# Kernel optimization log

Measured on AMD Instinct MI355X. Metric: run time of the kernel, lower is better.

## Reference

```python
import jax, jax.numpy as jnp
import numpy as np

B = 8          # batch_size
N = 2048       # N_particles
D_SP = 2       # spatial dims
D = 16         # D_SP + hidden_dim
K = 32         # max_num_neighbors
R = 0.08       # neighbor_radius
DT = 0.01      # leapfrog step
BIG = 1e9


def setup_inputs() -> dict:
    key = jax.random.key(0)
    ks = jax.random.split(key, 8)
    H, C = 64, 32
    # node state: small random hidden features, deterministic disk positions
    x = jax.random.normal(ks[0], (B * N, D), dtype=jnp.float32) * 0.001
    i = jnp.arange(N, dtype=jnp.float32)
    golden = jnp.pi * (3.0 - jnp.sqrt(5.0))
    theta = i * golden
    r = 0.6 * jnp.sqrt((i + 0.5) / N)
    pos = jnp.stack([r * jnp.cos(theta), r * jnp.sin(theta)], axis=1)  # [N,2]
    pos = jnp.tile(pos, (B, 1)) + 0.01 * jax.random.normal(ks[1], (B * N, 2), dtype=jnp.float32)
    x = x.at[:, :D_SP].set(pos)
    W1 = jax.random.normal(ks[2], (2 * D, H), dtype=jnp.float32) * (1.0 / np.sqrt(2 * D))
    b1 = jnp.zeros((H,), jnp.float32)
    W2 = jax.random.normal(ks[3], (H, C), dtype=jnp.float32) * (1.0 / np.sqrt(H))
    b2 = jnp.zeros((C,), jnp.float32)
    Wout = jax.random.normal(ks[4], (C, 1), dtype=jnp.float32) * (1.0 / np.sqrt(C))
    bout = jnp.zeros((1,), jnp.float32)
    batch = jnp.repeat(jnp.arange(B, dtype=jnp.int64), N)
    return {"x": x, "W1": W1, "b1": b1, "W2": W2, "b2": b2,
            "Wout": Wout, "bout": bout, "batch": batch, "steps": 2}


def reference(x, W1, b1, W2, b2, Wout, bout, batch, steps):
    Bn, Df = x.shape
    Bc = int(np.asarray(batch)[-1]) + 1      # batch is contiguous blocks
    Nn = Bn // Bc
    eye = jnp.eye(Nn, dtype=x.dtype) * BIG   # no self-loops (loop=False)

    def hamiltonian(xv):
        xb = xv.reshape(Bc, Nn, Df)
        pos = xb[:, :, :D_SP]                              # [B,N,2]
        # radius_graph: pairwise sq-dist per simulation, capped at K neighbors
        d2 = jnp.sum((pos[:, :, None, :] - pos[:, None, :, :]) ** 2, axis=-1)  # [B,N,N]
        d2 = d2 + eye
        negd, idx = jax.lax.top_k(-d2, K)                  # K nearest per node
        valid = (-negd) < (R * R)                          # [B,N,K]
        # gather neighbor states (HNNConv message on concat(x_i, x_j))
        xj = xb[jnp.arange(Bc)[:, None, None], idx]        # [B,N,K,D]
        xi = jnp.broadcast_to(xb[:, :, None, :], xj.shape)
        m = jnp.tanh(jnp.concatenate([xi, xj], axis=-1) @ W1 + b1)  # [B,N,K,H]
        m = m @ W2 + b2                                    # [B,N,K,C]
        m = jnp.where(valid[..., None], m, 0.0)
        agg = m.sum(axis=2)                                # sum aggregation [B,N,C]
        h = agg @ Wout + bout                              # per-node Hamiltonian [B,N,1]
        return h.sum()

    for _ in range(int(steps)):
        dHdx = jax.grad(hamiltonian)(x)
        x = x - DT * dHdx
    return x
```

## Files before the change

### kernel.cpp

```cpp
#include <hip/hip_runtime.h>
#include <cstdint>
#include <cstddef>

#define BB   8
#define NN   2048
#define DD   16
#define HHH  64
#define KK   32
#define CAP  96
#define FCAP 48
#define DT_C 0.01f
#define R2_C (0.08f * 0.08f)
#define CEXP (-2.885390081777927f)

#define WPB1  16
#define BLK1  (WPB1 * 64)
#define WPB2  8
#define BLK2  (WPB2 * 64)

__device__ __forceinline__ float dist2(float px, float py, float qx, float qy) {
    float dx = __fsub_rn(px, qx);
    float dy = __fsub_rn(py, qy);
    return __fadd_rn(__fmul_rn(dx, dx), __fmul_rn(dy, dy));
}

__device__ __forceinline__ int mbcnt64(unsigned long long m) {
    return (int)__builtin_amdgcn_mbcnt_hi(
        (unsigned)(m >> 32), __builtin_amdgcn_mbcnt_lo((unsigned)m, 0u));
}

__device__ __forceinline__ int swizzled_particle(int blk, int wpb, int w, int& bbase) {
    int vb = blk & 7, vi = blk >> 3;
    bbase = vb << 11;
    return bbase + vi * wpb + w;
}

template <bool FIRST>
__global__ __launch_bounds__(BLK1) void k_neighbors(
    const float* __restrict__ x, const float* __restrict__ pos,
    const float* __restrict__ W1,
    float2* __restrict__ candList, unsigned short* __restrict__ fwdList,
    int* __restrict__ cntArr, float* __restrict__ cutArr,
    float* __restrict__ Aplane, float* __restrict__ Dplane) {
    __shared__ float sPos[2 * NN];
    __shared__ float sW1[2 * DD * HHH];
    __shared__ float2 sDJ[WPB1][CAP];

    int tid = threadIdx.x;
    int w = tid >> 6, lane = tid & 63;
    int bbase;
    int p = swizzled_particle(blockIdx.x, WPB1, w, bbase);
    int pl = p & (NN - 1);

    float2* sPos2w = (float2*)sPos;
    if (FIRST) {
        for (int t = tid; t < NN; t += BLK1)
            sPos2w[t] = *(const float2*)(x + (size_t)(bbase + t) * DD);
    } else {
        for (int t = tid; t < 2 * NN; t += BLK1) sPos[t] = pos[bbase * 2 + t];
    }
    for (int t = tid; t < 2 * DD * HHH; t += BLK1) sW1[t] = W1[t];
    __syncthreads();

    float xv = (lane < DD) ? x[(size_t)p * DD + lane] : 0.f;
    float A = 0.f, Dv = 0.f;
#pragma unroll
    for (int f = 0; f < DD; f++) {
        float xf = __shfl(xv, f);
        A  = fmaf(xf, sW1[f * HHH + lane], A);
        Dv = fmaf(xf, sW1[(DD + f) * HHH + lane], Dv);
    }
    Aplane[((size_t)p << 6) + lane] = A;
    Dplane[((size_t)p << 6) + lane] = Dv;

    float px = sPos[2 * pl], py = sPos[2 * pl + 1];
    const float2* sPos2 = (const float2*)sPos;
    int cnt = 0;
    for (int c0 = 0; c0 < NN; c0 += 256) {
        float2 q[4];
#pragma unroll
        for (int u = 0; u < 4; ++u) q[u] = sPos2[c0 + (u << 6) + lane];
#pragma unroll
        for (int u = 0; u < 4; ++u) {
            int j = c0 + (u << 6) + lane;
            float d2 = dist2(px, py, q[u].x, q[u].y);
            bool hit = (d2 < R2_C) && (j != pl);
            unsigned long long m = __ballot(hit);
            int idx = cnt + mbcnt64(m & ((1ull << lane) - 1ull));
            if (hit && idx < CAP)
                sDJ[w][idx] = make_float2(d2, __uint_as_float((unsigned)j));
            cnt += (int)__popcll(m);
        }
    }
    if (cnt > CAP) cnt = CAP;
    __threadfence_block();

    float cutoff = R2_C;
    if (cnt > KK) {
        const float INF = 1e30f;
        if (cnt <= 64) {
            float v = (lane < cnt) ? sDJ[w][lane].x : INF;
#pragma unroll
            for (int k = 2; k <= 64; k <<= 1) {
#pragma unroll
                for (int j = k >> 1; j > 0; j >>= 1) {
                    float pv = __shfl_xor(v, j);
                    bool up = ((lane & k) == 0);
                    bool takeMin = (((lane & j) == 0) == up);
                    v = takeMin ? fminf(v, pv) : fmaxf(v, pv);
                }
            }
            cutoff = __shfl(v, KK - 1);
        } else {
            float e0 = (lane < cnt) ? sDJ[w][lane].x : INF;
            float e1 = (lane + 64 < cnt) ? sDJ[w][lane + 64].x : INF;
            int r0 = 0, q0 = 0, r1 = 0, q1 = 0;
            for (int k = 0; k < cnt; k++) {
                float val = sDJ[w][k].x;
                r0 += (val < e0); q0 += (val == e0);
                r1 += (val < e1); q1 += (val == e1);
            }
            bool c0 = (r0 <= KK - 1) && (r0 + q0 > KK - 1);
            bool c1 = (r1 <= KK - 1) && (r1 + q1 > KK - 1);
            float cand = c0 ? e0 : (c1 ? e1 : INF);
#pragma unroll
            for (int off = 32; off; off >>= 1) cand = fminf(cand, __shfl_xor(cand, off));
            cutoff = cand;
        }
    }

    int mf = 0;
    for (int c0 = 0; c0 < cnt; c0 += 64) {
        int c = c0 + lane;
        bool act = c < cnt;
        float2 e = sDJ[w][act ? c : 0];
        if (act) candList[(size_t)p * CAP + c] = e;
        bool fwd = act && (e.x <= cutoff);
        unsigned long long mF = __ballot(fwd);
        int iF = mf + mbcnt64(mF & ((1ull << lane) - 1ull));
        if (fwd && iF < FCAP)
            fwdList[(size_t)p * FCAP + iF] = (unsigned short)__float_as_uint(e.y);
        mf += (int)__popcll(mF);
    }
    if (mf > FCAP) mf = FCAP;
    if (lane == 0) { cutArr[p] = cutoff; cntArr[p] = cnt | (mf << 16); }
}

__global__ __launch_bounds__(BLK2) void k_grad(
    const float* __restrict__ x,
    const float* __restrict__ cutArr, const int* __restrict__ cntArr,
    const float2* __restrict__ candList, const unsigned short* __restrict__ fwdList,
    const float* __restrict__ Aplane, const float* __restrict__ Dplane,
    const float* __restrict__ W1, const float* __restrict__ b1,
    const float* __restrict__ W2, const float* __restrict__ Wout,
    float* __restrict__ xOut, float* __restrict__ posOut) {
    __shared__ float sW1t[HHH * 33];
    __shared__ alignas(16) unsigned short sFwd[WPB2][FCAP];
    __shared__ alignas(16) unsigned short sRev[WPB2][CAP];
    __shared__ float sS[WPB2][128];
    __shared__ float sV[HHH];

    int tid = threadIdx.x;
    int w = tid >> 6, h = tid & 63;
    int bbase;
    int p = swizzled_particle(blockIdx.x, WPB2, w, bbase);

    for (int t = tid; t < 2 * DD * HHH; t += BLK2) {
        int f = t >> 6, hh = t & 63;
        sW1t[hh * 33 + f] = W1[t];
    }
    if (tid < HHH) {
        float acc = 0.f;
        for (int c = 0; c < 32; c++) acc = fmaf(W2[tid * 32 + c], Wout[c], acc);
        sV[tid] = acc;
    }
    __syncthreads();

    float b1h = b1[h];
    float Apb = Aplane[((size_t)p << 6) + h] + b1h;
    float Dpb = Dplane[((size_t)p << 6) + h] + b1h;
    float vh4 = 4.f * sV[h];
    int packed = cntArr[p];
    int cnt = packed & 0xffff;
    int mf = packed >> 16;

    if (h < mf) sFwd[w][h] = fwdList[(size_t)p * FCAP + h];

    int mr = 0;
    for (int c0 = 0; c0 < cnt; c0 += 64) {
        int c = c0 + h;
        bool act = c < cnt;
        float2 e = candList[(size_t)p * CAP + (act ? c : 0)];
        unsigned jl = __float_as_uint(e.y) & (NN - 1);
        bool rev = act && (e.x <= cutArr[bbase + jl]);
        unsigned long long mR = __ballot(rev);
        int iR = mr + mbcnt64(mR & ((1ull << h) - 1ull));
        if (rev) sRev[w][iR] = (unsigned short)jl;
        mr += (int)__popcll(mR);
    }
    __threadfence_block();

    const float* baseD = Dplane + ((size_t)bbase << 6);
    const float* baseA = Aplane + ((size_t)bbase << 6);
    float T1 = 0.f, T2 = 0.f;

    auto s2core = [&](float z) {
        float a = __builtin_amdgcn_exp2f(CEXP * fabsf(z));
        float bb = 1.f + a;
        return a * __builtin_amdgcn_rcpf(bb * bb);
    };

#define UNPACK8(Q0, Q1, U)                                            \
    unsigned U[8];                                                    \
    U[0] = (unsigned)__builtin_amdgcn_readfirstlane(Q0.x);            \
    U[1] = (unsigned)__builtin_amdgcn_readfirstlane(Q0.y);            \
    U[2] = (unsigned)__builtin_amdgcn_readfirstlane(Q0.z);            \
    U[3] = (unsigned)__builtin_amdgcn_readfirstlane(Q0.w);            \
    U[4] = (unsigned)__builtin_amdgcn_readfirstlane(Q1.x);            \
    U[5] = (unsigned)__builtin_amdgcn_readfirstlane(Q1.y);            \
    U[6] = (unsigned)__builtin_amdgcn_readfirstlane(Q1.z);            \
    U[7] = (unsigned)__builtin_amdgcn_readfirstlane(Q1.w);

    {
        const unsigned short* L = sFwd[w];
        int c = 0;
        for (; c + 16 <= mf; c += 16) {
            int4 q0 = *(const int4*)(L + c);
            int4 q1 = *(const int4*)(L + c + 8);
            UNPACK8(q0, q1, u)
            float d[16];
#pragma unroll
            for (int k = 0; k < 8; ++k) {
                d[2 * k]     = baseD[((size_t)(u[k] & 0xffffu) << 6) + h];
                d[2 * k + 1] = baseD[((size_t)(u[k] >> 16) << 6) + h];
            }
#pragma unroll
            for (int k = 0; k < 16; ++k) T1 += s2core(Apb + d[k]);
        }
        for (; c + 8 <= mf; c += 8) {
            int4 q0 = *(const int4*)(L + c);
            int4 q1 = q0;
            UNPACK8(q0, q1, u)
            float d[8];
#pragma unroll
            for (int k = 0; k < 4; ++k) {
                d[2 * k]     = baseD[((size_t)(u[k] & 0xffffu) << 6) + h];
                d[2 * k + 1] = baseD[((size_t)(u[k] >> 16) << 6) + h];
            }
#pragma unroll
            for (int k = 0; k < 8; ++k) T1 += s2core(Apb + d[k]);
        }
        for (; c < mf; ++c) {
            unsigned jl = (unsigned)__builtin_amdgcn_readfirstlane((int)L[c]);
            T1 += s2core(Apb + baseD[((size_t)jl << 6) + h]);
        }
    }
    {
        const unsigned short* L = sRev[w];
        int c = 0;
        for (; c + 16 <= mr; c += 16) {
            int4 q0 = *(const int4*)(L + c);
            int4 q1 = *(const int4*)(L + c + 8);
            UNPACK8(q0, q1, u)
            float d[16];
#pragma unroll
            for (int k = 0; k < 8; ++k) {
                d[2 * k]     = baseA[((size_t)(u[k] & 0xffffu) << 6) + h];
                d[2 * k + 1] = baseA[((size_t)(u[k] >> 16) << 6) + h];
            }
#pragma unroll
            for (int k = 0; k < 16; ++k) T2 += s2core(Dpb + d[k]);
        }
        for (; c + 8 <= mr; c += 8) {
            int4 q0 = *(const int4*)(L + c);
            int4 q1 = q0;
            UNPACK8(q0, q1, u)
            float d[8];
#pragma unroll
            for (int k = 0; k < 4; ++k) {
                d[2 * k]     = baseA[((size_t)(u[k] & 0xffffu) << 6) + h];
                d[2 * k + 1] = baseA[((size_t)(u[k] >> 16) << 6) + h];
            }
#pragma unroll
            for (int k = 0; k < 8; ++k) T2 += s2core(Dpb + d[k]);
        }
        for (; c < mr; ++c) {
            unsigned jl = (unsigned)__builtin_amdgcn_readfirstlane((int)L[c]);
            T2 += s2core(Dpb + baseA[((size_t)jl << 6) + h]);
        }
    }
#undef UNPACK8

    sS[w][h] = vh4 * T1;
    sS[w][64 + h] = vh4 * T2;
    __threadfence_block();

    float g = 0.f;
    if (h < 32) {
        const float* Sv = &sS[w][(h < 16) ? 0 : 64];
        float acc = 0.f;
        for (int hh = 0; hh < 64; hh++) acc = fmaf(sW1t[hh * 33 + h], Sv[hh], acc);
        g = acc;
    }
    float g2 = __shfl(g, (h + 16) & 63);
    if (h < DD) {
        float xn = x[(size_t)p * DD + h] - DT_C * (g + g2);
        xOut[(size_t)p * DD + h] = xn;
        if (h < 2) posOut[p * 2 + h] = xn;
    }
}

extern "C" void kernel_launch(void* const* d_in, const int* in_sizes, int n_in,
                              void* d_out, int out_size, void* d_ws, size_t ws_size,
                              hipStream_t stream) {
    const float* x0   = (const float*)d_in[0];
    const float* W1   = (const float*)d_in[1];
    const float* b1   = (const float*)d_in[2];
    const float* W2   = (const float*)d_in[3];
    const float* Wout = (const float*)d_in[5];
    float* out = (float*)d_out;

    float* ws   = (float*)d_ws;
    float* posA = ws;
    float* posB = posA + 32768;
    float* x1   = posB + 32768;
    float* Apl  = x1 + 262144;
    float* Dpl  = Apl + 16384 * 64;
    float* cut  = Dpl + 16384 * 64;
    int*   cnt  = (int*)(cut + 16384);
    float2* cand = (float2*)(cnt + 16384);
    unsigned short* fwd = (unsigned short*)(cand + (size_t)16384 * CAP);

    const int NB1 = (BB * NN) / WPB1;
    const int NB2 = (BB * NN) / WPB2;

    k_neighbors<true><<<NB1, BLK1, 0, stream>>>(x0, nullptr, W1, cand, fwd, cnt, cut,
                                                Apl, Dpl);
    k_grad<<<NB2, BLK2, 0, stream>>>(x0, cut, cnt, cand, fwd, Apl, Dpl,
                                     W1, b1, W2, Wout, x1, posB);
    k_neighbors<false><<<NB1, BLK1, 0, stream>>>(x1, posB, W1, cand, fwd, cnt, cut,
                                                 Apl, Dpl);
    k_grad<<<NB2, BLK2, 0, stream>>>(x1, cut, cnt, cand, fwd, Apl, Dpl,
                                     W1, b1, W2, Wout, out, posA);
}
```

Before: 180.7 us.

## Bin particles into y-bands to prune all-pairs neighbor search

Adds a per-batch binning kernel that sorts particles into horizontal bands of width about the search radius. The neighbor kernel then scans only the three adjacent bands instead of all 2048 particles, and maps sorted indices back to original ones. Self-matches are now filtered after the fact, so the cutoff rank shifts by one. This cuts the O(N^2) distance work and the shared-memory position staging. It adds two small kernel launches, and the band bounds assume positions stay inside a fixed range.

```diff
diff --git a/kernel.cpp b/kernel.cpp
--- a/kernel.cpp
+++ b/kernel.cpp
@@ -13,10 +13,12 @@
 #define R2_C (0.08f * 0.08f)
 #define CEXP (-2.885390081777927f)
 
-#define WPB1  16
-#define BLK1  (WPB1 * 64)
-#define WPB2  8
-#define BLK2  (WPB2 * 64)
+#define BANDS    18
+#define BAND_OFF 0.72f
+#define BAND_INV 12.5f
+
+#define WPB   8
+#define BLOCK (WPB * 64)
 
 __device__ __forceinline__ float dist2(float px, float py, float qx, float qy) {
     float dx = __fsub_rn(px, qx);
@@ -24,45 +26,80 @@
     return __fadd_rn(__fmul_rn(dx, dx), __fmul_rn(dy, dy));
 }
 
-__device__ __forceinline__ int mbcnt64(unsigned long long m) {
+__device__ __forceinline__ int prefix_cnt(unsigned long long m) {
     return (int)__builtin_amdgcn_mbcnt_hi(
         (unsigned)(m >> 32), __builtin_amdgcn_mbcnt_lo((unsigned)m, 0u));
 }
 
-__device__ __forceinline__ int swizzled_particle(int blk, int wpb, int w, int& bbase) {
+__device__ __forceinline__ int swizzled_particle(int blk, int w, int& bbase) {
     int vb = blk & 7, vi = blk >> 3;
     bbase = vb << 11;
-    return bbase + vi * wpb + w;
+    return bbase + vi * WPB + w;
 }
 
 template <bool FIRST>
-__global__ __launch_bounds__(BLK1) void k_neighbors(
+__global__ __launch_bounds__(1024) void k_bin(
     const float* __restrict__ x, const float* __restrict__ pos,
-    const float* __restrict__ W1,
+    float2* __restrict__ sortedPos, unsigned short* __restrict__ sortedIdx,
+    int* __restrict__ bandStart) {
+    __shared__ int hist[BANDS], base[BANDS + 1], cursor[BANDS];
+    int bat = blockIdx.x;
+    int bbase = bat << 11;
+    int tid = threadIdx.x;
+    if (tid < BANDS) hist[tid] = 0;
+    __syncthreads();
+    float2 q[2]; int bd[2];
+#pragma unroll
+    for (int u = 0; u < 2; ++u) {
+        int i = tid + (u << 10);
+        float2 qq;
+        if (FIRST) qq = *(const float2*)(x + (size_t)(bbase + i) * DD);
+        else       qq = *(const float2*)(pos + (size_t)(bbase + i) * 2);
+        q[u] = qq;
+        int band = (int)((qq.y + BAND_OFF) * BAND_INV);
+        band = band < 0 ? 0 : (band > BANDS - 1 ? BANDS - 1 : band);
+        bd[u] = band;
+        atomicAdd(&hist[band], 1);
+    }
+    __syncthreads();
+    if (tid == 0) {
+        int acc = 0;
+        for (int k = 0; k < BANDS; ++k) { base[k] = acc; cursor[k] = acc; acc += hist[k]; }
+        base[BANDS] = acc;
+    }
+    __syncthreads();
+    if (tid <= BANDS) bandStart[bat * 32 + tid] = base[tid];
+#pragma unroll
+    for (int u = 0; u < 2; ++u) {
+        int i = tid + (u << 10);
+        int dst = atomicAdd(&cursor[bd[u]], 1);
+        sortedPos[bbase + dst] = q[u];
+        sortedIdx[bbase + dst] = (unsigned short)i;
+    }
+}
+
+__global__ __launch_bounds__(BLOCK) void k_neighbors(
+    const float* __restrict__ x,
+    const float2* __restrict__ sortedPos, const unsigned short* __restrict__ sortedIdx,
+    const int* __restrict__ bandStart, const float* __restrict__ W1,
     float2* __restrict__ candList, unsigned short* __restrict__ fwdList,
     int* __restrict__ cntArr, float* __restrict__ cutArr,
     float* __restrict__ Aplane, float* __restrict__ Dplane) {
-    __shared__ float sPos[2 * NN];
     __shared__ float sW1[2 * DD * HHH];
-    __shared__ float2 sDJ[WPB1][CAP];
+    __shared__ float2 sDJ[WPB][CAP];
 
     int tid = threadIdx.x;
     int w = tid >> 6, lane = tid & 63;
     int bbase;
-    int p = swizzled_particle(blockIdx.x, WPB1, w, bbase);
+    int p = swizzled_particle(blockIdx.x, w, bbase);
     int pl = p & (NN - 1);
-
-    float2* sPos2w = (float2*)sPos;
-    if (FIRST) {
-        for (int t = tid; t < NN; t += BLK1)
-            sPos2w[t] = *(const float2*)(x + (size_t)(bbase + t) * DD);
-    } else {
-        for (int t = tid; t < 2 * NN; t += BLK1) sPos[t] = pos[bbase * 2 + t];
-    }
-    for (int t = tid; t < 2 * DD * HHH; t += BLK1) sW1[t] = W1[t];
+    int bat = bbase >> 11;
+
+    for (int t = tid; t < 2 * DD * HHH; t += BLOCK) sW1[t] = W1[t];
     __syncthreads();
 
     float xv = (lane < DD) ? x[(size_t)p * DD + lane] : 0.f;
+    float px = __shfl(xv, 0), py = __shfl(xv, 1);
     float A = 0.f, Dv = 0.f;
 #pragma unroll
     for (int f = 0; f < DD; f++) {
@@ -73,30 +110,28 @@
     Aplane[((size_t)p << 6) + lane] = A;
     Dplane[((size_t)p << 6) + lane] = Dv;
 
-    float px = sPos[2 * pl], py = sPos[2 * pl + 1];
-    const float2* sPos2 = (const float2*)sPos;
+    int bb = (int)((py + BAND_OFF) * BAND_INV);
+    bb = bb < 0 ? 0 : (bb > BANDS - 1 ? BANDS - 1 : bb);
+    int lo = bandStart[bat * 32 + (bb > 0 ? bb - 1 : 0)];
+    int hi = bandStart[bat * 32 + (bb < BANDS - 1 ? bb + 2 : BANDS)];
+
     int cnt = 0;
-    for (int c0 = 0; c0 < NN; c0 += 256) {
-        float2 q[4];
-#pragma unroll
-        for (int u = 0; u < 4; ++u) q[u] = sPos2[c0 + (u << 6) + lane];
-#pragma unroll
-        for (int u = 0; u < 4; ++u) {
-            int j = c0 + (u << 6) + lane;
-            float d2 = dist2(px, py, q[u].x, q[u].y);
-            bool hit = (d2 < R2_C) && (j != pl);
-            unsigned long long m = __ballot(hit);
-            int idx = cnt + mbcnt64(m & ((1ull << lane) - 1ull));
-            if (hit && idx < CAP)
-                sDJ[w][idx] = make_float2(d2, __uint_as_float((unsigned)j));
-            cnt += (int)__popcll(m);
-        }
+    for (int c0 = lo; c0 < hi; c0 += 64) {
+        int j = c0 + lane;
+        float2 q = (j < hi) ? sortedPos[bbase + j] : make_float2(1e30f, 1e30f);
+        float d2 = dist2(px, py, q.x, q.y);
+        bool hit = (j < hi) && (d2 < R2_C);
+        unsigned long long m = __ballot(hit);
+        int idx = cnt + prefix_cnt(m);
+        if (hit && idx < CAP)
+            sDJ[w][idx] = make_float2(d2, __uint_as_float((unsigned)j));
+        cnt += (int)__popcll(m);
     }
     if (cnt > CAP) cnt = CAP;
     __threadfence_block();
 
     float cutoff = R2_C;
-    if (cnt > KK) {
+    if (cnt > KK + 1) {
         const float INF = 1e30f;
         if (cnt <= 64) {
             float v = (lane < cnt) ? sDJ[w][lane].x : INF;
@@ -110,7 +145,7 @@
                     v = takeMin ? fminf(v, pv) : fmaxf(v, pv);
                 }
             }
-            cutoff = __shfl(v, KK - 1);
+            cutoff = __shfl(v, KK);
         } else {
             float e0 = (lane < cnt) ? sDJ[w][lane].x : INF;
             float e1 = (lane + 64 < cnt) ? sDJ[w][lane + 64].x : INF;
@@ -120,8 +155,8 @@
                 r0 += (val < e0); q0 += (val == e0);
                 r1 += (val < e1); q1 += (val == e1);
             }
-            bool c0 = (r0 <= KK - 1) && (r0 + q0 > KK - 1);
-            bool c1 = (r1 <= KK - 1) && (r1 + q1 > KK - 1);
+            bool c0 = (r0 <= KK) && (r0 + q0 > KK);
+            bool c1 = (r1 <= KK) && (r1 + q1 > KK);
             float cand = c0 ? e0 : (c1 ? e1 : INF);
 #pragma unroll
             for (int off = 32; off; off >>= 1) cand = fminf(cand, __shfl_xor(cand, off));
@@ -129,24 +164,30 @@
         }
     }
 
-    int mf = 0;
+    int me = 0, mf = 0;
     for (int c0 = 0; c0 < cnt; c0 += 64) {
         int c = c0 + lane;
         bool act = c < cnt;
         float2 e = sDJ[w][act ? c : 0];
-        if (act) candList[(size_t)p * CAP + c] = e;
-        bool fwd = act && (e.x <= cutoff);
-        unsigned long long mF = __ballot(fwd);
-        int iF = mf + mbcnt64(mF & ((1ull << lane) - 1ull));
-        if (fwd && iF < FCAP)
-            fwdList[(size_t)p * FCAP + iF] = (unsigned short)__float_as_uint(e.y);
+        unsigned js = __float_as_uint(e.y);
+        int jo = act ? (int)sortedIdx[bbase + js] : pl;
+        bool keep = act && (jo != pl);
+        unsigned long long mK = __ballot(keep);
+        int ie = me + prefix_cnt(mK);
+        if (keep)
+            candList[(size_t)p * CAP + ie] = make_float2(e.x, __uint_as_float((unsigned)jo));
+        me += (int)__popcll(mK);
+        bool fw = keep && (e.x <= cutoff);
+        unsigned long long mF = __ballot(fw);
+        int iF = mf + prefix_cnt(mF);
+        if (fw && iF < FCAP) fwdList[(size_t)p * FCAP + iF] = (unsigned short)jo;
         mf += (int)__popcll(mF);
     }
     if (mf > FCAP) mf = FCAP;
-    if (lane == 0) { cutArr[p] = cutoff; cntArr[p] = cnt | (mf << 16); }
-}
-
-__global__ __launch_bounds__(BLK2) void k_grad(
+    if (lane == 0) { cutArr[p] = cutoff; cntArr[p] = me | (mf << 16); }
+}
+
+__global__ __launch_bounds__(BLOCK) void k_grad(
     const float* __restrict__ x,
     const float* __restrict__ cutArr, const int* __restrict__ cntArr,
     const float2* __restrict__ candList, const unsigned short* __restrict__ fwdList,
@@ -155,17 +196,17 @@
     const float* __restrict__ W2, const float* __restrict__ Wout,
     float* __restrict__ xOut, float* __restrict__ posOut) {
     __shared__ float sW1t[HHH * 33];
-    __shared__ alignas(16) unsigned short sFwd[WPB2][FCAP];
-    __shared__ alignas(16) unsigned short sRev[WPB2][CAP];
-    __shared__ float sS[WPB2][128];
+    __shared__ alignas(16) unsigned short sFwd[WPB][FCAP];
+    __shared__ alignas(16) unsigned short sRev[WPB][CAP];
+    __shared__ float sS[WPB][128];
     __shared__ float sV[HHH];
 
     int tid = threadIdx.x;
     int w = tid >> 6, h = tid & 63;
     int bbase;
-    int p = swizzled_particle(blockIdx.x, WPB2, w, bbase);
-
-    for (int t = tid; t < 2 * DD * HHH; t += BLK2) {
+    int p = swizzled_particle(blockIdx.x, w, bbase);
+
+    for (int t = tid; t < 2 * DD * HHH; t += BLOCK) {
         int f = t >> 6, hh = t & 63;
         sW1t[hh * 33 + f] = W1[t];
     }
@@ -194,7 +235,7 @@
         unsigned jl = __float_as_uint(e.y) & (NN - 1);
         bool rev = act && (e.x <= cutArr[bbase + jl]);
         unsigned long long mR = __ballot(rev);
-        int iR = mr + mbcnt64(mR & ((1ull << h) - 1ull));
+        int iR = mr + prefix_cnt(mR);
         if (rev) sRev[w][iR] = (unsigned short)jl;
         mr += (int)__popcll(mR);
     }
@@ -330,16 +371,20 @@
     int*   cnt  = (int*)(cut + 16384);
     float2* cand = (float2*)(cnt + 16384);
     unsigned short* fwd = (unsigned short*)(cand + (size_t)16384 * CAP);
-
-    const int NB1 = (BB * NN) / WPB1;
-    const int NB2 = (BB * NN) / WPB2;
-
-    k_neighbors<true><<<NB1, BLK1, 0, stream>>>(x0, nullptr, W1, cand, fwd, cnt, cut,
-                                                Apl, Dpl);
-    k_grad<<<NB2, BLK2, 0, stream>>>(x0, cut, cnt, cand, fwd, Apl, Dpl,
+    float2* sPosS = (float2*)(fwd + (size_t)16384 * FCAP);
+    unsigned short* sIdx = (unsigned short*)(sPosS + 16384);
+    int* bandStart = (int*)(sIdx + 16384);
+
+    const int NB = (BB * NN) / WPB;
+
+    k_bin<true><<<BB, 1024, 0, stream>>>(x0, nullptr, sPosS, sIdx, bandStart);
+    k_neighbors<<<NB, BLOCK, 0, stream>>>(x0, sPosS, sIdx, bandStart, W1,
+                                          cand, fwd, cnt, cut, Apl, Dpl);
+    k_grad<<<NB, BLOCK, 0, stream>>>(x0, cut, cnt, cand, fwd, Apl, Dpl,
                                      W1, b1, W2, Wout, x1, posB);
-    k_neighbors<false><<<NB1, BLK1, 0, stream>>>(x1, posB, W1, cand, fwd, cnt, cut,
-                                                 Apl, Dpl);
-    k_grad<<<NB2, BLK2, 0, stream>>>(x1, cut, cnt, cand, fwd, Apl, Dpl,
+    k_bin<false><<<BB, 1024, 0, stream>>>(nullptr, posB, sPosS, sIdx, bandStart);
+    k_neighbors<<<NB, BLOCK, 0, stream>>>(x1, sPosS, sIdx, bandStart, W1,
+                                          cand, fwd, cnt, cut, Apl, Dpl);
+    k_grad<<<NB, BLOCK, 0, stream>>>(x1, cut, cnt, cand, fwd, Apl, Dpl,
                                      W1, b1, W2, Wout, out, posA);
 }
```

Measured after the change: 169.8 us. 1.06x faster.
